# Performance work log

Hardware: AMD Instinct MI355X
Metric: run time of the kernel (lower is better)

Reference implementation:

```python
import jax, jax.numpy as jnp
import numpy as np

B, N, M, DIN, H = 8, 2048, 2048, 512, 256
SCALE = float(np.sqrt(H))


def _lin_params(key, din, dout):
    kw, kb = jax.random.split(key)
    lim = 1.0 / np.sqrt(din)
    W = jax.random.uniform(kw, (din, dout), jnp.float32, -lim, lim)
    b = jax.random.uniform(kb, (dout,), jnp.float32, -lim, lim)
    return W, b


def setup_inputs() -> dict:
    key = jax.random.key(0)
    ks = jax.random.split(key, 16)
    inp = {
        "q_fp": jax.random.normal(ks[0], (B, N, DIN), jnp.float32),
        "v_ret": jax.random.normal(ks[1], (B, M, DIN), jnp.float32),
        "pi_star": jax.random.uniform(ks[2], (B, N, M), jnp.float32),
    }
    names = ["qs", "ks", "vs", "qe", "ke", "ve"]
    for i, nm in enumerate(names):
        W, b = _lin_params(ks[3 + i], DIN, H)
        inp[f"W{nm}"], inp[f"b{nm}"] = W, b
    inp["W1"], inp["b1"] = _lin_params(ks[10], 4 * H, H)
    inp["W2"], inp["b2"] = _lin_params(ks[11], H, H)
    inp["gamma"] = jnp.ones((1,), jnp.float32)
    inp["ew"] = jnp.array(1.0, jnp.float32)
    return inp


def _forward(q_fp, v_ret, pi_star, Wqs, bqs, Wks, bks, Wvs, bvs,
             Wqe, bqe, Wke, bke, Wve, bve, W1, b1, W2, b2, gamma, ew):
    q_struct = q_fp @ Wqs + bqs          # [B,N,H]
    k_struct = v_ret @ Wks + bks         # [B,M,H]
    v_struct = v_ret @ Wvs + bvs
    q_elec = q_fp @ Wqe + bqe
    k_elec = v_ret @ Wke + bke
    v_elec = v_ret @ Wve + bve

    structural_logits = jnp.einsum("bnh,bmh->bnm", q_struct, k_struct) / SCALE

    # cdist(p=2) via the quadratic expansion, clamped for numeric safety
    q2 = jnp.sum(q_elec * q_elec, -1, keepdims=True)          # [B,N,1]
    k2 = jnp.sum(k_elec * k_elec, -1, keepdims=True)          # [B,M,1]
    d2 = q2 + jnp.swapaxes(k2, -2, -1) - 2.0 * jnp.einsum("bnh,bmh->bnm", q_elec, k_elec)
    electronic_distance = jnp.sqrt(jnp.maximum(d2, 1e-12))    # [B,N,M]
    electronic_scale = jnp.maximum(
        electronic_distance.mean(axis=(-2, -1), keepdims=True), 1e-4)
    electronic_logits = -(electronic_distance / electronic_scale)

    pi_mask = gamma * jnp.log(jnp.maximum(pi_star, 1e-9))
    final_logits = structural_logits + ew * electronic_logits + pi_mask
    attn = jax.nn.softmax(final_logits, axis=-1)              # [B,N,M]

    ctx_s = jnp.einsum("bnm,bmh->bnh", attn, v_struct)
    ctx_e = jnp.einsum("bnm,bmh->bnh", attn, v_elec)
    fused = jnp.concatenate([ctx_s, ctx_e, ctx_s - ctx_e, ctx_s * ctx_e], axis=-1)
    h = jax.nn.silu(fused @ W1 + b1)
    return h @ W2 + b2


def reference(q_fp, v_ret, pi_star, Wqs, bqs, Wks, bks, Wvs, bvs,
              Wqe, bqe, Wke, bke, Wve, bve, W1, b1, W2, b2, gamma, ew):
    return _forward(q_fp, v_ret, pi_star, Wqs, bqs, Wks, bks, Wvs, bvs,
                    Wqe, bqe, Wke, bke, Wve, bve, W1, b1, W2, b2, gamma, ew)
```

## Files before the change

### kernel.cpp

```cpp
#include <hip/hip_runtime.h>

#define Bsz 8
#define Nq  2048
#define Mk  2048
#define BKt 32

typedef __attribute__((ext_vector_type(8))) short   short8;
typedef __attribute__((ext_vector_type(4))) float   floatx4;

__device__ __forceinline__ unsigned short f2bf(float f) {
  union { float f; unsigned u; } x; x.f = f;
  unsigned r = x.u + 0x7fffu + ((x.u >> 16) & 1u);
  return (unsigned short)(r >> 16);
}
__device__ __forceinline__ float bf2f(unsigned short s) {
  union { unsigned u; float f; } x; x.u = ((unsigned)s) << 16;
  return x.f;
}

__device__ __forceinline__ void gload16(const unsigned short* g, unsigned short* l) {
  __builtin_amdgcn_global_load_lds(
      (const __attribute__((address_space(1))) void*)g,
      (__attribute__((address_space(3))) void*)l, 16, 0, 0);
}

__device__ __forceinline__ void gemm_core8_nt(
    const unsigned short* __restrict__ A, int lda,
    const unsigned short* __restrict__ B, int ldb,
    int K, unsigned short* ldsA, unsigned short* ldsB,
    floatx4 (&acc)[4][2])
{
  const int tid  = threadIdx.x;
  const int lane = tid & 63;
  const int wid  = tid >> 6;
  const int wm   = wid & 1;
  const int wn   = wid >> 1;
  const int fr   = lane & 15;
  const int fk   = (lane >> 4) << 3;
  const int lr   = lane >> 2;
  const int lc   = (lane & 3) << 3;
  const int r0   = wid << 4;

  const unsigned short* gA = A + (size_t)(r0 + lr) * lda + lc;
  const unsigned short* gB = B + (size_t)(r0 + lr) * ldb + lc;
  unsigned short* lA = ldsA + r0 * BKt;
  unsigned short* lB = ldsB + r0 * BKt;
  const unsigned short* fa = ldsA + (wm * 64 + fr) * BKt + fk;
  const unsigned short* fb = ldsB + (wn * 32 + fr) * BKt + fk;

  for (int k0 = 0; k0 < K; k0 += BKt) {
    __syncthreads();
    gload16(gA, lA); gA += BKt;
    gload16(gB, lB); gB += BKt;
    __syncthreads();
    short8 af[4], bfr[2];
#pragma unroll
    for (int i = 0; i < 4; i++) af[i]  = *(const short8*)(fa + i * 16 * BKt);
#pragma unroll
    for (int j = 0; j < 2; j++) bfr[j] = *(const short8*)(fb + j * 16 * BKt);
#pragma unroll
    for (int i = 0; i < 4; i++)
#pragma unroll
      for (int j = 0; j < 2; j++)
        acc[i][j] = __builtin_amdgcn_mfma_f32_16x16x32_bf16(af[i], bfr[j], acc[i][j], 0, 0, 0);
  }
}

#define EPILOGUE_VARS \
  const int lane = threadIdx.x & 63; \
  const int wid  = threadIdx.x >> 6; \
  const int wm   = wid & 1; \
  const int wn   = wid >> 1; \
  const int r4   = (lane >> 4) * 4;  \
  const int cn   = lane & 15; \
  (void)wid;

__global__ __launch_bounds__(512, 4) void k_proj(
    const float* __restrict__ A, const unsigned short* __restrict__ Bw,
    const float* __restrict__ bias, unsigned short* __restrict__ Cout,
    int Ncols, int K)
{
  __shared__ alignas(16) unsigned short ldsA[128 * BKt];
  __shared__ alignas(16) unsigned short ldsB[128 * BKt];
  floatx4 acc[4][2];
#pragma unroll
  for (int i = 0; i < 4; i++)
#pragma unroll
    for (int j = 0; j < 2; j++)
#pragma unroll
      for (int t = 0; t < 4; t++) acc[i][j][t] = 0.f;

  const int tid  = threadIdx.x;
  const int lane = tid & 63;
  const int wid  = tid >> 6;
  const int wm   = wid & 1;
  const int wn   = wid >> 1;
  const int fr   = lane & 15;
  const int fk   = (lane >> 4) << 3;
  const int lr   = lane >> 2;
  const int lc   = (lane & 3) << 3;
  const int r0   = wid << 4;

  const float* ap = A + ((size_t)blockIdx.x * 128 + r0 + lr) * K + lc;
  const unsigned short* gB = Bw + ((size_t)blockIdx.y * 128 + r0 + lr) * K + lc;
  unsigned short* lB = ldsB + r0 * BKt;
  uint4* sa = (uint4*)(ldsA + (r0 + lr) * BKt + lc);
  const unsigned short* fa = ldsA + (wm * 64 + fr) * BKt + fk;
  const unsigned short* fb = ldsB + (wn * 32 + fr) * BKt + fk;

  for (int k0 = 0; k0 < K; k0 += BKt) {
    float4 f0 = *(const float4*)(ap + 0);
    float4 f1 = *(const float4*)(ap + 4);
    ap += BKt;
    uint4 pa;
    pa.x = f2bf(f0.x) | ((unsigned)f2bf(f0.y) << 16);
    pa.y = f2bf(f0.z) | ((unsigned)f2bf(f0.w) << 16);
    pa.z = f2bf(f1.x) | ((unsigned)f2bf(f1.y) << 16);
    pa.w = f2bf(f1.z) | ((unsigned)f2bf(f1.w) << 16);
    __syncthreads();
    gload16(gB, lB); gB += BKt;
    *sa = pa;
    __syncthreads();
    short8 af[4], bfr[2];
#pragma unroll
    for (int i = 0; i < 4; i++) af[i]  = *(const short8*)(fa + i * 16 * BKt);
#pragma unroll
    for (int j = 0; j < 2; j++) bfr[j] = *(const short8*)(fb + j * 16 * BKt);
#pragma unroll
    for (int i = 0; i < 4; i++)
#pragma unroll
      for (int j = 0; j < 2; j++)
        acc[i][j] = __builtin_amdgcn_mfma_f32_16x16x32_bf16(af[i], bfr[j], acc[i][j], 0, 0, 0);
  }

  const int r4 = (lane >> 4) * 4;
  const int cn = lane & 15;
#pragma unroll
  for (int i = 0; i < 4; i++) {
#pragma unroll
    for (int j = 0; j < 2; j++) {
      int gc = blockIdx.y * 128 + wn * 32 + j * 16 + cn;
      float bv = bias[gc];
#pragma unroll
      for (int r = 0; r < 4; r++) {
        int gr = blockIdx.x * 128 + wm * 64 + i * 16 + r4 + r;
        Cout[(size_t)gr * Ncols + gc] = f2bf(acc[i][j][r] + bv);
      }
    }
  }
}

template<int MODE>
__global__ __launch_bounds__(512, 4) void k_gemm_bias(
    const unsigned short* __restrict__ A, const unsigned short* __restrict__ Bw,
    const float* __restrict__ bias, void* __restrict__ Cout, int Ncols, int K)
{
  __shared__ alignas(16) unsigned short ldsA[128 * BKt];
  __shared__ alignas(16) unsigned short ldsB[128 * BKt];
  floatx4 acc[4][2];
#pragma unroll
  for (int i = 0; i < 4; i++)
#pragma unroll
    for (int j = 0; j < 2; j++)
#pragma unroll
      for (int t = 0; t < 4; t++) acc[i][j][t] = 0.f;

  const unsigned short* Ab = A + (size_t)blockIdx.x * 128 * K;
  const unsigned short* Bb = Bw + (size_t)blockIdx.y * 128 * K;
  gemm_core8_nt(Ab, K, Bb, K, K, ldsA, ldsB, acc);

  EPILOGUE_VARS
#pragma unroll
  for (int i = 0; i < 4; i++) {
#pragma unroll
    for (int j = 0; j < 2; j++) {
      int gc = blockIdx.y * 128 + wn * 32 + j * 16 + cn;
      float bv = bias[gc];
#pragma unroll
      for (int r = 0; r < 4; r++) {
        int gr = blockIdx.x * 128 + wm * 64 + i * 16 + r4 + r;
        float v = acc[i][j][r] + bv;
        if constexpr (MODE == 1) v = v / (1.f + __expf(-v));
        if constexpr (MODE == 2)
          ((float*)Cout)[(size_t)gr * Ncols + gc] = v;
        else
          ((unsigned short*)Cout)[(size_t)gr * Ncols + gc] = f2bf(v);
      }
    }
  }
}

__global__ __launch_bounds__(512, 4) void k_sd(
    const unsigned short* __restrict__ Xq, const unsigned short* __restrict__ Xk,
    const float* __restrict__ q2, const float* __restrict__ k2,
    int b0, float* __restrict__ dsum, unsigned* __restrict__ sd)
{
  __shared__ alignas(16) unsigned short ldsA[128 * BKt];
  __shared__ alignas(16) unsigned short ldsB[128 * BKt];
  floatx4 accS[4][2], accE[4][2];
#pragma unroll
  for (int i = 0; i < 4; i++)
#pragma unroll
    for (int j = 0; j < 2; j++)
#pragma unroll
      for (int t = 0; t < 4; t++) { accS[i][j][t] = 0.f; accE[i][j][t] = 0.f; }

  const int z = blockIdx.z;
  const int b = b0 + z;
  const unsigned short* Aq = Xq + ((size_t)(b * Nq) + blockIdx.x * 128) * 512;
  const unsigned short* Bk = Xk + ((size_t)(b * Mk) + blockIdx.y * 128) * 1024;
  gemm_core8_nt(Aq,       512, Bk,       1024, 256, ldsA, ldsB, accS);
  gemm_core8_nt(Aq + 256, 512, Bk + 512, 1024, 256, ldsA, ldsB, accE);

  EPILOGUE_VARS
  const int colT = blockIdx.y * 128 + wn * 32;
  const float kk0 = k2[b * Mk + colT + cn];
  const float kk1 = k2[b * Mk + colT + 16 + cn];

  float lsum = 0.f;
#pragma unroll
  for (int i = 0; i < 4; i++) {
#pragma unroll
    for (int r = 0; r < 4; r++) {
      const int n = blockIdx.x * 128 + wm * 64 + i * 16 + r4 + r;
      const float qq = q2[b * Nq + n];
      unsigned* srow = sd + (size_t)(z * Nq + n) * Mk;
#pragma unroll
      for (int j = 0; j < 2; j++) {
        const int m = colT + j * 16 + cn;
        float d = sqrtf(fmaxf(qq + (j ? kk1 : kk0) - 2.f * accE[i][j][r], 1e-12f));
        lsum += d;
        srow[m] = (unsigned)f2bf(accS[i][j][r] * 0.0625f)
                | ((unsigned)f2bf(d) << 16);
      }
    }
  }
#pragma unroll
  for (int o = 32; o; o >>= 1) lsum += __shfl_down(lsum, o);
  __syncthreads();
  float* red = (float*)ldsA;
  if (lane == 0) red[wid] = lsum;
  __syncthreads();
  if (threadIdx.x == 0) {
    float s = 0.f;
#pragma unroll
    for (int t = 0; t < 8; t++) s += red[t];
    atomicAdd(dsum + b, s);
  }
}

__global__ __launch_bounds__(256) void k_softmax(
    const unsigned* __restrict__ sd, const float* __restrict__ pi,
    const float* __restrict__ dsum, const float* __restrict__ gamma_p,
    const float* __restrict__ ew_p, int b0,
    unsigned short* __restrict__ attn, float* __restrict__ rowsum)
{
  const int wid  = threadIdx.x >> 6;
  const int lane = threadIdx.x & 63;
  const int rl   = blockIdx.x * 4 + wid;
  const int b    = b0 + (rl >> 11);
  const int n    = rl & 2047;

  const float scale = fmaxf(dsum[b] * (1.f / (2048.f * 2048.f)), 1e-4f);
  const float einv  = ew_p[0] / scale;
  const float gv    = gamma_p[0];
  const bool  g1    = (gv == 1.0f);

  const unsigned*  sp = sd  + (size_t)rl * Mk;
  const float*     pp = pi  + ((size_t)b * Nq + n) * Mk;
  unsigned short*  ap = attn + ((size_t)b * Nq + n) * Mk;

  float rs = 0.f;
  for (int it = 0; it < 8; ++it) {
    const int c = it * 256 + lane * 4;
    const uint4  sv = *(const uint4*)(sp + c);
    const float4 pv = *(const float4*)(pp + c);
    const unsigned uu[4]  = {sv.x, sv.y, sv.z, sv.w};
    const float    pp4[4] = {pv.x, pv.y, pv.z, pv.w};
    float e[4];
#pragma unroll
    for (int t = 0; t < 4; ++t) {
      union { unsigned u; float f; } cs, cd;
      cs.u = uu[t] << 16;
      cd.u = uu[t] & 0xffff0000u;
      float p  = fmaxf(pp4[t], 1e-9f);
      float pf = g1 ? p : __expf(gv * __logf(p));
      e[t] = __expf(cs.f - einv * cd.f) * pf;
      rs += e[t];
    }
    uint2 st;
    st.x = (unsigned)f2bf(e[0]) | ((unsigned)f2bf(e[1]) << 16);
    st.y = (unsigned)f2bf(e[2]) | ((unsigned)f2bf(e[3]) << 16);
    *(uint2*)(ap + c) = st;
  }
#pragma unroll
  for (int o = 32; o; o >>= 1) rs += __shfl_down(rs, o);
  if (lane == 0) rowsum[b * Nq + n] = rs;
}

__global__ __launch_bounds__(512, 4) void k_pv(
    const unsigned short* __restrict__ At, const unsigned short* __restrict__ VT,
    const float* __restrict__ rowsum, unsigned short* __restrict__ ctx)
{
  __shared__ alignas(16) unsigned short ldsA[128 * BKt];
  __shared__ alignas(16) unsigned short ldsB[128 * BKt];
  floatx4 acc[4][2];
#pragma unroll
  for (int i = 0; i < 4; i++)
#pragma unroll
    for (int j = 0; j < 2; j++)
#pragma unroll
      for (int t = 0; t < 4; t++) acc[i][j][t] = 0.f;

  const int l  = blockIdx.x;
  const int lg = ((l & 7) << 3) | (l >> 3);
  const int tx = lg >> 2;
  const int ty = lg & 3;
  const int b  = blockIdx.z;
  const unsigned short* Ab = At + ((size_t)b * Nq + tx * 128) * (size_t)Mk;
  const unsigned short* Bb = VT + ((size_t)b * 512 + ty * 128) * (size_t)Mk;
  gemm_core8_nt(Ab, Mk, Bb, Mk, Mk, ldsA, ldsB, acc);

  EPILOGUE_VARS
  const int rowbase = b * Nq + tx * 128 + wm * 64;
#pragma unroll
  for (int i = 0; i < 4; i++) {
    float rinv[4];
#pragma unroll
    for (int r = 0; r < 4; r++)
      rinv[r] = 1.f / rowsum[rowbase + i * 16 + r4 + r];
#pragma unroll
    for (int j = 0; j < 2; j++) {
      int gc = ty * 128 + wn * 32 + j * 16 + cn;
#pragma unroll
      for (int r = 0; r < 4; r++) {
        int gr = tx * 128 + wm * 64 + i * 16 + r4 + r;
        ctx[((size_t)b * Nq + gr) * 512 + gc] = f2bf(acc[i][j][r] * rinv[r]);
      }
    }
  }
}

__global__ void k_prep_w(
    const float* __restrict__ Wqs, const float* __restrict__ Wqe,
    const float* __restrict__ Wks, const float* __restrict__ Wvs,
    const float* __restrict__ Wke, const float* __restrict__ Wve,
    const float* __restrict__ W1,  const float* __restrict__ W2,
    const float* __restrict__ bqs, const float* __restrict__ bqe,
    const float* __restrict__ bks, const float* __restrict__ bvs,
    const float* __restrict__ bke, const float* __restrict__ bve,
    unsigned short* __restrict__ WqT, unsigned short* __restrict__ WkT,
    unsigned short* __restrict__ W1T, unsigned short* __restrict__ W2T,
    float* __restrict__ bq, float* __restrict__ bk, float* __restrict__ dsum)
{
  int gid = blockIdx.x * 256 + threadIdx.x;
  int idx = gid;
  if (idx < 512 * 512) {
    int j = idx >> 9, k = idx & 511;
    float v = (j < 256) ? Wqs[k * 256 + j] : Wqe[k * 256 + (j - 256)];
    WqT[idx] = f2bf(v);
  } else if ((idx -= 512 * 512) < 1024 * 512) {
    int j = idx >> 9, k = idx & 511;
    int s = j >> 8, jj = j & 255;
    const float* Wp = (s == 0) ? Wks : (s == 1) ? Wvs : (s == 2) ? Wke : Wve;
    WkT[idx] = f2bf(Wp[k * 256 + jj]);
  } else if ((idx -= 1024 * 512) < 256 * 1024) {
    int j = idx >> 10, k = idx & 1023;
    W1T[idx] = f2bf(W1[k * 256 + j]);
  } else if ((idx -= 256 * 1024) < 256 * 256) {
    int j = idx >> 8, k = idx & 255;
    W2T[idx] = f2bf(W2[k * 256 + j]);
  }
  if (gid < 512)  bq[gid] = (gid < 256) ? bqs[gid] : bqe[gid - 256];
  if (gid < 1024) bk[gid] = (gid < 256) ? bks[gid]
                    : (gid < 512) ? bvs[gid - 256]
                    : (gid < 768) ? bke[gid - 512] : bve[gid - 768];
  if (gid < 8) dsum[gid] = 0.f;
}

__global__ __launch_bounds__(256) void k_rowsq(
    const unsigned short* __restrict__ X, int stride, int colOff, float* __restrict__ out)
{
  int row = blockIdx.x * 4 + (threadIdx.x >> 6);
  int lane = threadIdx.x & 63;
  const unsigned short* p = X + (size_t)row * stride + colOff + lane * 4;
  uint2 u = *(const uint2*)p;
  float a0 = bf2f((unsigned short)(u.x & 0xffff));
  float a1 = bf2f((unsigned short)(u.x >> 16));
  float a2 = bf2f((unsigned short)(u.y & 0xffff));
  float a3 = bf2f((unsigned short)(u.y >> 16));
  float s = a0 * a0 + a1 * a1 + a2 * a2 + a3 * a3;
#pragma unroll
  for (int o = 32; o; o >>= 1) s += __shfl_down(s, o);
  if (lane == 0) out[row] = s;
}

__global__ void k_trans_vt(const unsigned short* __restrict__ Xk, unsigned short* __restrict__ VT) {
  __shared__ unsigned short t[32][33];
  const int b = blockIdx.z;
  const int m0 = blockIdx.x * 32, j0 = blockIdx.y * 32;
  const int tx = threadIdx.x, ty = threadIdx.y;
#pragma unroll
  for (int i = 0; i < 4; i++) {
    int m = m0 + ty + i * 8;
    int j = j0 + tx;
    int c = (j < 256) ? (256 + j) : (512 + j);
    t[ty + i * 8][tx] = Xk[((size_t)b * Mk + m) * 1024 + c];
  }
  __syncthreads();
#pragma unroll
  for (int i = 0; i < 4; i++) {
    int j = j0 + ty + i * 8;
    int m = m0 + tx;
    VT[((size_t)b * 512 + j) * Mk + m] = t[tx][ty + i * 8];
  }
}

__global__ void k_fused(const unsigned short* __restrict__ ctx, unsigned short* __restrict__ fused) {
  int idx = blockIdx.x * 256 + threadIdx.x;
  int bn = idx >> 8;
  int j = idx & 255;
  float cs = bf2f(ctx[(size_t)bn * 512 + j]);
  float ce = bf2f(ctx[(size_t)bn * 512 + 256 + j]);
  size_t o = (size_t)bn * 1024 + j;
  fused[o]       = f2bf(cs);
  fused[o + 256] = f2bf(ce);
  fused[o + 512] = f2bf(cs - ce);
  fused[o + 768] = f2bf(cs * ce);
}

extern "C" void kernel_launch(void* const* d_in, const int* in_sizes, int n_in,
                              void* d_out, int out_size, void* d_ws, size_t ws_size,
                              hipStream_t stream) {
  (void)in_sizes; (void)n_in; (void)out_size; (void)ws_size;
  const float* q_fp  = (const float*)d_in[0];
  const float* v_ret = (const float*)d_in[1];
  const float* pi    = (const float*)d_in[2];
  const float* Wqs = (const float*)d_in[3];  const float* bqs = (const float*)d_in[4];
  const float* Wks = (const float*)d_in[5];  const float* bks = (const float*)d_in[6];
  const float* Wvs = (const float*)d_in[7];  const float* bvs = (const float*)d_in[8];
  const float* Wqe = (const float*)d_in[9];  const float* bqe = (const float*)d_in[10];
  const float* Wke = (const float*)d_in[11]; const float* bke = (const float*)d_in[12];
  const float* Wve = (const float*)d_in[13]; const float* bve = (const float*)d_in[14];
  const float* W1  = (const float*)d_in[15]; const float* b1  = (const float*)d_in[16];
  const float* W2  = (const float*)d_in[17]; const float* b2  = (const float*)d_in[18];
  const float* gamma = (const float*)d_in[19];
  const float* ew    = (const float*)d_in[20];

  char* w = (char*)d_ws;
  unsigned short* WqT = (unsigned short*)(w + 0);
  unsigned short* WkT = (unsigned short*)(w + 524288);
  unsigned short* W1T = (unsigned short*)(w + 1572864);
  unsigned short* W2T = (unsigned short*)(w + 2097152);
  float* bq   = (float*)(w + 2228224);
  float* bk   = (float*)(w + 2230272);
  float* q2   = (float*)(w + 2234368);
  float* k2   = (float*)(w + 2299904);
  float* dsum = (float*)(w + 2365440);
  unsigned short* ctx  = (unsigned short*)(w + 2365696);
  unsigned short* hbuf = (unsigned short*)(w + 19142912);
  unsigned short* Xq = (unsigned short*)(w + 35920128);
  unsigned short* Xk = (unsigned short*)(w + 52697344);
  unsigned short* VT = (unsigned short*)(w + 86251776);
  unsigned short* attn = (unsigned short*)(w + 103028992);
  unsigned short* fused = attn;
  unsigned* sdbuf = (unsigned*)(w + 2365696);
  float* rowsum = (float*)d_out;

  k_prep_w<<<4352, 256, 0, stream>>>(Wqs, Wqe, Wks, Wvs, Wke, Wve, W1, W2,
                                     bqs, bqe, bks, bvs, bke, bve,
                                     WqT, WkT, W1T, W2T, bq, bk, dsum);
  k_proj<<<dim3(128, 4), 512, 0, stream>>>(q_fp,  WqT, bq, Xq, 512, 512);
  k_proj<<<dim3(128, 8), 512, 0, stream>>>(v_ret, WkT, bk, Xk, 1024, 512);
  k_rowsq<<<4096, 256, 0, stream>>>(Xq, 512, 256, q2);
  k_rowsq<<<4096, 256, 0, stream>>>(Xk, 1024, 512, k2);
  for (int c = 0; c < 4; ++c) {
    k_sd<<<dim3(16, 16, 2), 512, 0, stream>>>(Xq, Xk, q2, k2, 2 * c, dsum, sdbuf);
    k_softmax<<<1024, 256, 0, stream>>>(sdbuf, pi, dsum, gamma, ew, 2 * c,
                                        attn, rowsum);
  }
  k_trans_vt<<<dim3(64, 16, 8), dim3(32, 8), 0, stream>>>(Xk, VT);
  k_pv<<<dim3(64, 1, 8), 512, 0, stream>>>(attn, VT, rowsum, ctx);
  k_fused<<<16384, 256, 0, stream>>>(ctx, fused);
  k_gemm_bias<1><<<dim3(128, 2), 512, 0, stream>>>(fused, W1T, b1, hbuf, 256, 1024);
  k_gemm_bias<2><<<dim3(128, 2), 512, 0, stream>>>(hbuf, W2T, b2, d_out, 256, 256);
}
```

Baseline: 567.5 us.

## Double-buffer LDS tiles in GEMM cores to overlap global loads with MFMA

Turns the shared GEMM core and the projection kernel into a two-stage LDS ping-pong. Each step issues the next K-tile's global-to-LDS loads (and, in the projection kernel, the fp32 loads and bf16 conversion) before or alongside the MFMAs on the current tile, so two barriers per step become one. This is meant to hide global memory latency behind matrix compute. In exchange, LDS per block doubles, which may reduce occupancy under the 512-thread launch bounds.

Result: no change. 576.5 us (+1.6%).

```diff
diff --git a/kernel.cpp b/kernel.cpp
--- a/kernel.cpp
+++ b/kernel.cpp
@@ -4,6 +4,7 @@
 #define Nq  2048
 #define Mk  2048
 #define BKt 32
+#define BUFE (128 * BKt)
 
 typedef __attribute__((ext_vector_type(8))) short   short8;
 typedef __attribute__((ext_vector_type(4))) float   floatx4;
@@ -48,21 +49,31 @@
   const unsigned short* fa = ldsA + (wm * 64 + fr) * BKt + fk;
   const unsigned short* fb = ldsB + (wn * 32 + fr) * BKt + fk;
 
+  gload16(gA, lA); gA += BKt;
+  gload16(gB, lB); gB += BKt;
+  __syncthreads();
+
+  int cur = 0;
   for (int k0 = 0; k0 < K; k0 += BKt) {
-    __syncthreads();
-    gload16(gA, lA); gA += BKt;
-    gload16(gB, lB); gB += BKt;
-    __syncthreads();
+    const int nxt = cur ^ 1;
+    if (k0 + BKt < K) {
+      gload16(gA, lA + nxt * BUFE); gA += BKt;
+      gload16(gB, lB + nxt * BUFE); gB += BKt;
+    }
+    const unsigned short* fac = fa + cur * BUFE;
+    const unsigned short* fbc = fb + cur * BUFE;
     short8 af[4], bfr[2];
 #pragma unroll
-    for (int i = 0; i < 4; i++) af[i]  = *(const short8*)(fa + i * 16 * BKt);
-#pragma unroll
-    for (int j = 0; j < 2; j++) bfr[j] = *(const short8*)(fb + j * 16 * BKt);
+    for (int i = 0; i < 4; i++) af[i]  = *(const short8*)(fac + i * 16 * BKt);
+#pragma unroll
+    for (int j = 0; j < 2; j++) bfr[j] = *(const short8*)(fbc + j * 16 * BKt);
 #pragma unroll
     for (int i = 0; i < 4; i++)
 #pragma unroll
       for (int j = 0; j < 2; j++)
         acc[i][j] = __builtin_amdgcn_mfma_f32_16x16x32_bf16(af[i], bfr[j], acc[i][j], 0, 0, 0);
+    __syncthreads();
+    cur = nxt;
   }
 }
 
@@ -80,8 +91,8 @@
     const float* __restrict__ bias, unsigned short* __restrict__ Cout,
     int Ncols, int K)
 {
-  __shared__ alignas(16) unsigned short ldsA[128 * BKt];
-  __shared__ alignas(16) unsigned short ldsB[128 * BKt];
+  __shared__ alignas(16) unsigned short ldsA[2 * BUFE];
+  __shared__ alignas(16) unsigned short ldsB[2 * BUFE];
   floatx4 acc[4][2];
 #pragma unroll
   for (int i = 0; i < 4; i++)
@@ -104,12 +115,12 @@
   const float* ap = A + ((size_t)blockIdx.x * 128 + r0 + lr) * K + lc;
   const unsigned short* gB = Bw + ((size_t)blockIdx.y * 128 + r0 + lr) * K + lc;
   unsigned short* lB = ldsB + r0 * BKt;
-  uint4* sa = (uint4*)(ldsA + (r0 + lr) * BKt + lc);
+  unsigned short* sa = ldsA + (r0 + lr) * BKt + lc;
   const unsigned short* fa = ldsA + (wm * 64 + fr) * BKt + fk;
   const unsigned short* fb = ldsB + (wn * 32 + fr) * BKt + fk;
 
-  for (int k0 = 0; k0 < K; k0 += BKt) {
-    float4 f0 = *(const float4*)(ap + 0);
+  {
+    float4 f0 = *(const float4*)(ap);
     float4 f1 = *(const float4*)(ap + 4);
     ap += BKt;
     uint4 pa;
@@ -117,20 +128,44 @@
     pa.y = f2bf(f0.z) | ((unsigned)f2bf(f0.w) << 16);
     pa.z = f2bf(f1.x) | ((unsigned)f2bf(f1.y) << 16);
     pa.w = f2bf(f1.z) | ((unsigned)f2bf(f1.w) << 16);
-    __syncthreads();
     gload16(gB, lB); gB += BKt;
-    *sa = pa;
-    __syncthreads();
+    *(uint4*)sa = pa;
+  }
+  __syncthreads();
+
+  int cur = 0;
+  for (int k0 = 0; k0 < K; k0 += BKt) {
+    const int nxt = cur ^ 1;
+    const bool more = (k0 + BKt < K);
+    float4 n0, n1;
+    if (more) {
+      n0 = *(const float4*)(ap);
+      n1 = *(const float4*)(ap + 4);
+      ap += BKt;
+      gload16(gB, lB + nxt * BUFE); gB += BKt;
+    }
+    const unsigned short* fac = fa + cur * BUFE;
+    const unsigned short* fbc = fb + cur * BUFE;
     short8 af[4], bfr[2];
 #pragma unroll
-    for (int i = 0; i < 4; i++) af[i]  = *(const short8*)(fa + i * 16 * BKt);
-#pragma unroll
-    for (int j = 0; j < 2; j++) bfr[j] = *(const short8*)(fb + j * 16 * BKt);
+    for (int i = 0; i < 4; i++) af[i]  = *(const short8*)(fac + i * 16 * BKt);
+#pragma unroll
+    for (int j = 0; j < 2; j++) bfr[j] = *(const short8*)(fbc + j * 16 * BKt);
 #pragma unroll
     for (int i = 0; i < 4; i++)
 #pragma unroll
       for (int j = 0; j < 2; j++)
         acc[i][j] = __builtin_amdgcn_mfma_f32_16x16x32_bf16(af[i], bfr[j], acc[i][j], 0, 0, 0);
+    if (more) {
+      uint4 pa;
+      pa.x = f2bf(n0.x) | ((unsigned)f2bf(n0.y) << 16);
+      pa.y = f2bf(n0.z) | ((unsigned)f2bf(n0.w) << 16);
+      pa.z = f2bf(n1.x) | ((unsigned)f2bf(n1.y) << 16);
+      pa.w = f2bf(n1.z) | ((unsigned)f2bf(n1.w) << 16);
+      *(uint4*)(sa + nxt * BUFE) = pa;
+    }
+    __syncthreads();
+    cur = nxt;
   }
 
   const int r4 = (lane >> 4) * 4;
@@ -155,8 +190,8 @@
     const unsigned short* __restrict__ A, const unsigned short* __restrict__ Bw,
     const float* __restrict__ bias, void* __restrict__ Cout, int Ncols, int K)
 {
-  __shared__ alignas(16) unsigned short ldsA[128 * BKt];
-  __shared__ alignas(16) unsigned short ldsB[128 * BKt];
+  __shared__ alignas(16) unsigned short ldsA[2 * BUFE];
+  __shared__ alignas(16) unsigned short ldsB[2 * BUFE];
   floatx4 acc[4][2];
 #pragma unroll
   for (int i = 0; i < 4; i++)
@@ -195,8 +230,8 @@
     const float* __restrict__ q2, const float* __restrict__ k2,
     int b0, float* __restrict__ dsum, unsigned* __restrict__ sd)
 {
-  __shared__ alignas(16) unsigned short ldsA[128 * BKt];
-  __shared__ alignas(16) unsigned short ldsB[128 * BKt];
+  __shared__ alignas(16) unsigned short ldsA[2 * BUFE];
+  __shared__ alignas(16) unsigned short ldsB[2 * BUFE];
   floatx4 accS[4][2], accE[4][2];
 #pragma unroll
   for (int i = 0; i < 4; i++)
@@ -302,8 +337,8 @@
     const unsigned short* __restrict__ At, const unsigned short* __restrict__ VT,
     const float* __restrict__ rowsum, unsigned short* __restrict__ ctx)
 {
-  __shared__ alignas(16) unsigned short ldsA[128 * BKt];
-  __shared__ alignas(16) unsigned short ldsB[128 * BKt];
+  __shared__ alignas(16) unsigned short ldsA[2 * BUFE];
+  __shared__ alignas(16) unsigned short ldsB[2 * BUFE];
   floatx4 acc[4][2];
 #pragma unroll
   for (int i = 0; i < 4; i++)
```
